# Kernel tuning notes

Measured on AMD Instinct MI355X. Metric: run time of the kernel, lower is better.

Reference implementation:

```python
import jax, jax.numpy as jnp
import numpy as np

E = 1024
BUCKET = 16
TAU = 0.75
ITERS = 8
SCALE = E ** -0.5
EPS = 1e-6


def _gumbel(rng, shape):
    u = jax.random.uniform(rng, shape, jnp.float32, 0.0, 1.0)
    return -jnp.log(-jnp.log(u + EPS) + EPS)


def _log_sinkhorn(log_alpha, n_iter):
    def body(i, la):
        la = la - jax.scipy.special.logsumexp(la, axis=-1, keepdims=True)
        la = la - jax.scipy.special.logsumexp(la, axis=-2, keepdims=True)
        return la
    return jnp.exp(jax.lax.fori_loop(0, n_iter, body, log_alpha))


def setup_inputs() -> dict:
    rng = jax.random.key(0)
    ks = jax.random.split(rng, 9)
    T, B, S = 4096, 8, 4096
    w = 0.02
    return {
        "query": jax.random.normal(ks[0], (T, B, E), jnp.float32),
        "key": jax.random.normal(ks[1], (S, B, E), jnp.float32),
        "value": jax.random.normal(ks[2], (S, B, E), jnp.float32),
        "wq": jax.random.normal(ks[3], (E, E), jnp.float32) * w,
        "bq": jnp.zeros((E,), jnp.float32),
        "wk": jax.random.normal(ks[4], (E, E), jnp.float32) * w,
        "bk": jnp.zeros((E,), jnp.float32),
        "wo": jax.random.normal(ks[5], (E, E), jnp.float32) * w,
        "bo": jnp.zeros((E,), jnp.float32),
    }


def reference(query, key, value, wq, bq, wk, bk, wo, bo):
    T, B, _ = query.shape
    S = key.shape[0]
    # projections (Linear: x @ W.T + b), move to (B, T, E)
    q = jnp.einsum('tbe,fe->btf', query, wq) + bq
    k = jnp.einsum('sbe,fe->bsf', key, wk) + bk
    v = jnp.transpose(value, (1, 0, 2))  # (B, S, E)
    nb, nkb = T // BUCKET, S // BUCKET
    # bucket aggregation: mean-pool q/k, flatten v buckets
    qb = q.reshape(B, nb, BUCKET, E).mean(axis=2)          # (B, nb, E)
    kb = k.reshape(B, nkb, BUCKET, E).mean(axis=2)         # (B, nkb, E)
    vb = v.reshape(B, nkb, BUCKET * E)                     # (B, nkb, BUCKET*E)
    # dot energy
    logits = jnp.einsum('bqe,bke->bqk', qb, kb) * SCALE    # (B, nb, nkb)
    log_alpha = logits
    # gumbel-sinkhorn (noise=True)
    g = _gumbel(jax.random.key(42), logits.shape)
    attn_weights = _log_sinkhorn((logits.astype(jnp.float32) + g) / TAU, ITERS)
    # attend on flattened buckets, then un-aggregate
    attn = jnp.einsum('bqk,bkd->bqd', attn_weights, vb)    # (B, nb, BUCKET*E)
    attn = attn.reshape(B, nb * BUCKET, E)
    attn = jnp.transpose(attn, (1, 0, 2))                  # (T, B, E)
    out = jnp.einsum('tbe,fe->tbf', attn, wo) + bo
    return out, attn_weights, log_alpha
```

## Files before the change

### kernel.cpp

```cpp
#include <hip/hip_runtime.h>


typedef float    f32x4 __attribute__((ext_vector_type(4)));
typedef _Float16 h4    __attribute__((ext_vector_type(4)));
typedef _Float16 h8    __attribute__((ext_vector_type(8)));

#define OUT_ELEMS 33554432
#define AW_ELEMS  524288

__device__ __forceinline__ void gload16(const void* g, void* l) {
  __builtin_amdgcn_global_load_lds((__attribute__((address_space(1))) void*)g,
                                   (__attribute__((address_space(3))) void*)l,
                                   16, 0, 0);
}

__global__ __launch_bounds__(256) void convw_k(const float* __restrict__ wq,
                                               const float* __restrict__ wk,
                                               const float* __restrict__ wo,
                                               _Float16* __restrict__ dst) {
  int which = blockIdx.y;
  const float* src = which == 0 ? wq : (which == 1 ? wk : wo);
  size_t idx = (size_t)blockIdx.x * 256 + threadIdx.x;
  f32x4 v = ((const f32x4*)src)[idx];
  ((h4*)(dst + (size_t)which * 1048576))[idx] = __builtin_convertvector(v, h4);
}

__global__ __launch_bounds__(256) void bucket_k(const float* __restrict__ q,
                                                const float* __restrict__ k,
                                                _Float16* __restrict__ qbar,
                                                _Float16* __restrict__ kbar) {
  const float* src = blockIdx.y ? k : q;
  _Float16* dst = blockIdx.y ? kbar : qbar;
  unsigned t = blockIdx.x * 256 + threadIdx.x;
  int e4 = t & 255, i = (t >> 8) & 255, b = t >> 16;
  const f32x4* p = (const f32x4*)(src + ((size_t)(i * 16) * 8 + b) * 1024) + e4;
  f32x4 acc = {0.f, 0.f, 0.f, 0.f};
  #pragma unroll
  for (int j = 0; j < 16; ++j) acc += p[j * 2048];
  acc *= 0.0625f;
  ((h4*)(dst + (size_t)(b * 256 + i) * 1024))[e4] = __builtin_convertvector(acc, h4);
}

__global__ __launch_bounds__(256) void vtrans_k(const float* __restrict__ v,
                                                _Float16* __restrict__ vt) {
  int bid = blockIdx.x;
  int kb = bid & 3, eb = (bid >> 2) & 15, j = (bid >> 6) & 15, b = bid >> 10;
  int k0 = kb * 64, e0 = eb * 64;
  __shared__ _Float16 tile[64][72];
  int t = threadIdx.x, r = t >> 2, qq = t & 3;
  const float* src = v + ((size_t)((k0 + r) * 16 + j) * 8 + b) * 1024 + e0;
  #pragma unroll
  for (int ii = 0; ii < 4; ++ii) {
    f32x4 x = ((const f32x4*)src)[qq + ii * 4];
    *(h4*)&tile[r][(qq + ii * 4) * 4] = __builtin_convertvector(x, h4);
  }
  __syncthreads();
  _Float16* dstp = vt + (((size_t)(b * 16 + j) * 1024 + e0 + r) * 256 + k0 + qq * 16);
  h8 o0, o1;
  #pragma unroll
  for (int kk = 0; kk < 8; ++kk) o0[kk] = tile[qq * 16 + kk][r];
  #pragma unroll
  for (int kk = 0; kk < 8; ++kk) o1[kk] = tile[qq * 16 + 8 + kk][r];
  *(h8*)dstp = o0;
  *(h8*)(dstp + 8) = o1;
}

__device__ __forceinline__ unsigned rotl32(unsigned x, int r) {
  return (x << r) | (x >> (32 - r));
}
__global__ __launch_bounds__(256) void gumbel_k(const float* __restrict__ logits,
                                                float* __restrict__ ebuf) {
  unsigned i = blockIdx.x * 256 + threadIdx.x;
  const unsigned k0 = 0u, k1 = 42u, k2 = 0u ^ 42u ^ 0x1BD11BDAu;
  unsigned x0 = 0u + k0, x1 = i + k1;
#define R4(a,b,c,d) \
  x0 += x1; x1 = rotl32(x1, a); x1 ^= x0; \
  x0 += x1; x1 = rotl32(x1, b); x1 ^= x0; \
  x0 += x1; x1 = rotl32(x1, c); x1 ^= x0; \
  x0 += x1; x1 = rotl32(x1, d); x1 ^= x0;
  R4(13,15,26,6)  x0 += k1; x1 += k2 + 1u;
  R4(17,29,16,24) x0 += k2; x1 += k0 + 2u;
  R4(13,15,26,6)  x0 += k0; x1 += k1 + 3u;
  R4(17,29,16,24) x0 += k1; x1 += k2 + 4u;
  R4(13,15,26,6)  x0 += k2; x1 += k0 + 5u;
#undef R4
  unsigned bits = x0 ^ x1;
  float u = __builtin_bit_cast(float, (bits >> 9) | 0x3f800000u) - 1.0f;
  float g = -logf(-logf(u + 1e-6f) + 1e-6f);
  ebuf[i] = __expf((logits[i] + g) / 0.75f);
}

__global__ __launch_bounds__(1024) void sink_rc_k(const float* __restrict__ ein,
                                                  float* __restrict__ attnw,
                                                  _Float16* __restrict__ wsh) {
  const int b = blockIdx.x;
  const int t = threadIdx.x;
  const int r = t >> 2, p = t & 3;
  const int k = t & 255, g = t >> 8;
  const float* Eb = ein + (size_t)b * 65536;
  const f32x4* Eb4 = (const f32x4*)Eb;

  __shared__ float ra[256];
  __shared__ float cb[256];
  __shared__ float part[4][256];
  if (t < 256) cb[t] = 1.0f;
  __syncthreads();

  const f32x4* cb4 = (const f32x4*)cb;

  for (int it = 0; it < 8; ++it) {
    float s = 0.f;
    #pragma unroll
    for (int i = 0; i < 16; ++i) {
      f32x4 e = Eb4[r * 64 + p * 16 + i];
      f32x4 c = cb4[p * 16 + i];
      f32x4 m = e * c;
      s += (m[0] + m[1]) + (m[2] + m[3]);
    }
    s += __shfl_xor(s, 1, 64);
    s += __shfl_xor(s, 2, 64);
    if (p == 0) ra[r] = 1.0f / s;
    __syncthreads();
    float s2 = 0.f;
    #pragma unroll 8
    for (int q2 = 0; q2 < 64; ++q2) {
      int row = g * 64 + q2;
      s2 += Eb[row * 256 + k] * ra[row];
    }
    part[g][k] = s2;
    __syncthreads();
    if (t < 256) {
      cb[t] = 1.0f / (part[0][t] + part[1][t] + part[2][t] + part[3][t]);
    }
    __syncthreads();
  }

  const float arow = ra[r];
  f32x4* aw = (f32x4*)(attnw + (size_t)b * 65536 + r * 256 + p * 64);
  h4* wh = (h4*)(wsh + (size_t)b * 65536 + r * 256 + p * 64);
  #pragma unroll
  for (int i = 0; i < 16; ++i) {
    f32x4 e = Eb4[r * 64 + p * 16 + i];
    f32x4 c = cb4[p * 16 + i];
    f32x4 w = e * c * arow;
    aw[i] = w;
    h4 hv;
    hv[0] = (_Float16)w[0]; hv[1] = (_Float16)w[1];
    hv[2] = (_Float16)w[2]; hv[3] = (_Float16)w[3];
    wh[i] = hv;
  }
}

template <int MODE>
__global__ __launch_bounds__(256) void gemm128(const _Float16* __restrict__ A,
                                               const _Float16* __restrict__ B,
                                               const float* __restrict__ bias,
                                               const float* __restrict__ bias2,
                                               void* __restrict__ out0,
                                               int K, int lda, int ldb) {
  const int tid = threadIdx.x, lane = tid & 63, w = tid >> 6;
  int bx = blockIdx.x, by = blockIdx.y, bz = blockIdx.z;
  if constexpr (MODE == 0) {
    int wid = ((bx & 7) << 4) + (bx >> 3);
    by = wid & 7; bx = wid >> 3;
  }
  if constexpr (MODE == 2) {
    int wid = ((bx & 7) << 8) + (bx >> 3);
    bz = wid >> 4; by = (wid >> 1) & 7; bx = wid & 1;
  }
  if constexpr (MODE == 3) {
    int wid = ((bx & 7) << 8) + (bx >> 3);
    by = wid & 7; bx = wid >> 3;
  }
  const int m0 = bx * 128, n0 = by * 128;
  const _Float16* Ab = A;
  const _Float16* Bb = B;
  const float* bs = bias;
  if constexpr (MODE == 0) {
    Ab += (size_t)bz * 2097152;
    Bb += (size_t)bz * 1048576;
    if (bz) bs = bias2;
  }
  if constexpr (MODE == 1) { Ab += (size_t)bz * 262144; Bb += (size_t)bz * 262144; }
  if constexpr (MODE == 2) { Ab += (size_t)(bz >> 4) * 65536; Bb += (size_t)bz * 262144; }
  __shared__ _Float16 lA[128 * 32];
  __shared__ _Float16 lB[128 * 32];
  f32x4 acc[4][4] = {};
  const int wm = (w >> 1) * 64, wn = (w & 1) * 64;
  const int fr = lane & 15, fk = (lane >> 4) * 8;
  const int q0 = tid, q1 = tid + 256;

  for (int kt = 0; kt < K; kt += 32) {
    __syncthreads();
    gload16(Ab + (size_t)(m0 + (q0 >> 2)) * lda + kt + (q0 & 3) * 8, &lA[(w * 64) * 8]);
    gload16(Ab + (size_t)(m0 + (q1 >> 2)) * lda + kt + (q1 & 3) * 8, &lA[(256 + w * 64) * 8]);
    gload16(Bb + (size_t)(n0 + (q0 >> 2)) * ldb + kt + (q0 & 3) * 8, &lB[(w * 64) * 8]);
    gload16(Bb + (size_t)(n0 + (q1 >> 2)) * ldb + kt + (q1 & 3) * 8, &lB[(256 + w * 64) * 8]);
    __syncthreads();
    h8 af[4], bf[4];
    #pragma unroll
    for (int i = 0; i < 4; ++i) {
      af[i] = *(const h8*)&lA[(wm + i * 16 + fr) * 32 + fk];
      bf[i] = *(const h8*)&lB[(wn + i * 16 + fr) * 32 + fk];
    }
    #pragma unroll
    for (int mi = 0; mi < 4; ++mi)
      #pragma unroll
      for (int ni = 0; ni < 4; ++ni)
        acc[mi][ni] = __builtin_amdgcn_mfma_f32_16x16x32_f16(af[mi], bf[ni], acc[mi][ni], 0, 0, 0);
  }

  const int er = (lane >> 4) * 4;
  #pragma unroll
  for (int mi = 0; mi < 4; ++mi) {
    #pragma unroll
    for (int ni = 0; ni < 4; ++ni) {
      #pragma unroll
      for (int r = 0; r < 4; ++r) {
        int row = m0 + wm + mi * 16 + er + r;
        int col = n0 + wn + ni * 16 + fr;
        float val = acc[mi][ni][r];
        if constexpr (MODE == 0) {
          ((_Float16*)out0)[(size_t)bz * 2097152 + (size_t)row * 1024 + col] =
              (_Float16)(val + bs[col]);
        } else if constexpr (MODE == 1) {
          ((float*)out0)[(size_t)bz * 65536 + row * 256 + col] = val * 0.03125f;
        } else if constexpr (MODE == 2) {
          int b = bz >> 4, j = bz & 15;
          ((_Float16*)out0)[((size_t)(b * 4096 + row * 16 + j)) * 1024 + col] = (_Float16)val;
        } else {
          int bb = row >> 12, t = row & 4095;
          ((float*)out0)[((size_t)t * 8 + bb) * 1024 + col] = val + bs[col];
        }
      }
    }
  }
}

extern "C" void kernel_launch(void* const* d_in, const int* in_sizes, int n_in,
                              void* d_out, int out_size, void* d_ws, size_t ws_size,
                              hipStream_t stream) {
  const float* query = (const float*)d_in[0];
  const float* key   = (const float*)d_in[1];
  const float* value = (const float*)d_in[2];
  const float* wq    = (const float*)d_in[3];
  const float* bq    = (const float*)d_in[4];
  const float* wk    = (const float*)d_in[5];
  const float* bk    = (const float*)d_in[6];
  const float* wo    = (const float*)d_in[7];
  const float* bo    = (const float*)d_in[8];

  float* out      = (float*)d_out;
  float* attnw    = out + OUT_ELEMS;
  float* logalpha = out + OUT_ELEMS + AW_ELEMS;

  char* ws = (char*)d_ws;
  const size_t MB = 1024 * 1024;
  _Float16* wqh   = (_Float16*)(ws + 0 * MB);
  _Float16* woh   = (_Float16*)(ws + 4 * MB);
  _Float16* qbar  = (_Float16*)(ws + 6 * MB);
  _Float16* kbar  = (_Float16*)(ws + 10 * MB);
  _Float16* qbh   = (_Float16*)(ws + 14 * MB);
  _Float16* kbh   = (_Float16*)(ws + 18 * MB);
  float*    ebuf  = (float*)(ws + 22 * MB);
  _Float16* wsh   = (_Float16*)(ws + 25 * MB);
  _Float16* vt    = (_Float16*)(ws + 26 * MB);
  _Float16* attnh = (_Float16*)(ws + 90 * MB);
  (void)in_sizes; (void)n_in; (void)out_size; (void)ws_size;

  convw_k<<<dim3(1024, 3), 256, 0, stream>>>(wq, wk, wo, wqh);
  bucket_k<<<dim3(2048, 2), 256, 0, stream>>>(query, key, qbar, kbar);
  vtrans_k<<<dim3(8192), 256, 0, stream>>>(value, vt);

  gemm128<0><<<dim3(128, 1, 2), 256, 0, stream>>>(qbar, wqh, bq, bk, qbh, 1024, 1024, 1024);
  gemm128<1><<<dim3(2, 2, 8), 256, 0, stream>>>(qbh, kbh, nullptr, nullptr, logalpha, 1024, 1024, 1024);

  gumbel_k<<<dim3(2048), 256, 0, stream>>>(logalpha, ebuf);
  sink_rc_k<<<dim3(8), 1024, 0, stream>>>(ebuf, attnw, wsh);

  gemm128<2><<<dim3(2048), 256, 0, stream>>>(wsh, vt, nullptr, nullptr, attnh, 256, 256, 256);
  gemm128<3><<<dim3(2048), 256, 0, stream>>>(attnh, woh, bo, nullptr, out, 1024, 1024, 1024);
}
```

Baseline: 377.9 us.

## Merge weight/bucket prep kernels and overlap V transpose with Sinkhorn

Fuses the weight-conversion and bucket-mean kernels into a single launch, and moves the V transpose into the Sinkhorn kernel as extra blocks. The Sinkhorn step runs on only 8 blocks, so the 2048 transpose blocks (four 256-thread sub-tiles per 1024-thread block) fill the otherwise idle CUs while it runs. This removes two launches and hides the transpose's memory traffic behind the latency-bound normalization. The cost is a larger shared allocation per block and a shared __syncthreads across the four sub-tiles.

```diff
diff --git a/kernel.cpp b/kernel.cpp
--- a/kernel.cpp
+++ b/kernel.cpp
@@ -14,55 +14,34 @@
                                    16, 0, 0);
 }
 
-__global__ __launch_bounds__(256) void convw_k(const float* __restrict__ wq,
-                                               const float* __restrict__ wk,
-                                               const float* __restrict__ wo,
-                                               _Float16* __restrict__ dst) {
-  int which = blockIdx.y;
-  const float* src = which == 0 ? wq : (which == 1 ? wk : wo);
-  size_t idx = (size_t)blockIdx.x * 256 + threadIdx.x;
-  f32x4 v = ((const f32x4*)src)[idx];
-  ((h4*)(dst + (size_t)which * 1048576))[idx] = __builtin_convertvector(v, h4);
-}
-
-__global__ __launch_bounds__(256) void bucket_k(const float* __restrict__ q,
-                                                const float* __restrict__ k,
-                                                _Float16* __restrict__ qbar,
-                                                _Float16* __restrict__ kbar) {
-  const float* src = blockIdx.y ? k : q;
-  _Float16* dst = blockIdx.y ? kbar : qbar;
-  unsigned t = blockIdx.x * 256 + threadIdx.x;
-  int e4 = t & 255, i = (t >> 8) & 255, b = t >> 16;
-  const f32x4* p = (const f32x4*)(src + ((size_t)(i * 16) * 8 + b) * 1024) + e4;
-  f32x4 acc = {0.f, 0.f, 0.f, 0.f};
-  #pragma unroll
-  for (int j = 0; j < 16; ++j) acc += p[j * 2048];
-  acc *= 0.0625f;
-  ((h4*)(dst + (size_t)(b * 256 + i) * 1024))[e4] = __builtin_convertvector(acc, h4);
-}
-
-__global__ __launch_bounds__(256) void vtrans_k(const float* __restrict__ v,
-                                                _Float16* __restrict__ vt) {
+__global__ __launch_bounds__(256) void cb_k(const float* __restrict__ wq,
+                                            const float* __restrict__ wk,
+                                            const float* __restrict__ wo,
+                                            _Float16* __restrict__ wdst,
+                                            const float* __restrict__ q,
+                                            const float* __restrict__ k,
+                                            _Float16* __restrict__ qbar,
+                                            _Float16* __restrict__ kbar) {
   int bid = blockIdx.x;
-  int kb = bid & 3, eb = (bid >> 2) & 15, j = (bid >> 6) & 15, b = bid >> 10;
-  int k0 = kb * 64, e0 = eb * 64;
-  __shared__ _Float16 tile[64][72];
-  int t = threadIdx.x, r = t >> 2, qq = t & 3;
-  const float* src = v + ((size_t)((k0 + r) * 16 + j) * 8 + b) * 1024 + e0;
-  #pragma unroll
-  for (int ii = 0; ii < 4; ++ii) {
-    f32x4 x = ((const f32x4*)src)[qq + ii * 4];
-    *(h4*)&tile[r][(qq + ii * 4) * 4] = __builtin_convertvector(x, h4);
-  }
-  __syncthreads();
-  _Float16* dstp = vt + (((size_t)(b * 16 + j) * 1024 + e0 + r) * 256 + k0 + qq * 16);
-  h8 o0, o1;
-  #pragma unroll
-  for (int kk = 0; kk < 8; ++kk) o0[kk] = tile[qq * 16 + kk][r];
-  #pragma unroll
-  for (int kk = 0; kk < 8; ++kk) o1[kk] = tile[qq * 16 + 8 + kk][r];
-  *(h8*)dstp = o0;
-  *(h8*)(dstp + 8) = o1;
+  if (bid < 3072) {
+    int which = bid >> 10;
+    const float* src = which == 0 ? wq : (which == 1 ? wk : wo);
+    size_t idx = (size_t)(bid & 1023) * 256 + threadIdx.x;
+    f32x4 v = ((const f32x4*)src)[idx];
+    ((h4*)(wdst + (size_t)which * 1048576))[idx] = __builtin_convertvector(v, h4);
+  } else {
+    int vb = bid - 3072;
+    const float* src = (vb >= 2048) ? k : q;
+    _Float16* dst = (vb >= 2048) ? kbar : qbar;
+    unsigned t = (unsigned)(vb & 2047) * 256 + threadIdx.x;
+    int e4 = t & 255, i = (t >> 8) & 255, b = t >> 16;
+    const f32x4* p = (const f32x4*)(src + ((size_t)(i * 16) * 8 + b) * 1024) + e4;
+    f32x4 acc = {0.f, 0.f, 0.f, 0.f};
+    #pragma unroll
+    for (int j = 0; j < 16; ++j) acc += p[j * 2048];
+    acc *= 0.0625f;
+    ((h4*)(dst + (size_t)(b * 256 + i) * 1024))[e4] = __builtin_convertvector(acc, h4);
+  }
 }
 
 __device__ __forceinline__ unsigned rotl32(unsigned x, int r) {
@@ -90,64 +69,89 @@
   ebuf[i] = __expf((logits[i] + g) / 0.75f);
 }
 
-__global__ __launch_bounds__(1024) void sink_rc_k(const float* __restrict__ ein,
-                                                  float* __restrict__ attnw,
-                                                  _Float16* __restrict__ wsh) {
-  const int b = blockIdx.x;
+__global__ __launch_bounds__(1024) void sinkvt_k(const float* __restrict__ ein,
+                                                 float* __restrict__ attnw,
+                                                 _Float16* __restrict__ wsh,
+                                                 const float* __restrict__ v,
+                                                 _Float16* __restrict__ vt) {
+  __shared__ __attribute__((aligned(16))) char smem[36864];
   const int t = threadIdx.x;
-  const int r = t >> 2, p = t & 3;
-  const int k = t & 255, g = t >> 8;
-  const float* Eb = ein + (size_t)b * 65536;
-  const f32x4* Eb4 = (const f32x4*)Eb;
-
-  __shared__ float ra[256];
-  __shared__ float cb[256];
-  __shared__ float part[4][256];
-  if (t < 256) cb[t] = 1.0f;
-  __syncthreads();
-
-  const f32x4* cb4 = (const f32x4*)cb;
-
-  for (int it = 0; it < 8; ++it) {
-    float s = 0.f;
+  if (blockIdx.x < 8) {
+    const int b = blockIdx.x;
+    const int r = t >> 2, p = t & 3;
+    const int k = t & 255, g = t >> 8;
+    const float* Eb = ein + (size_t)b * 65536;
+    const f32x4* Eb4 = (const f32x4*)Eb;
+    float* ra = (float*)smem;
+    float* cb = ra + 256;
+    float (*part)[256] = (float (*)[256])(cb + 256);
+    if (t < 256) cb[t] = 1.0f;
+    __syncthreads();
+    const f32x4* cb4 = (const f32x4*)cb;
+
+    for (int it = 0; it < 8; ++it) {
+      float s = 0.f;
+      #pragma unroll
+      for (int i = 0; i < 16; ++i) {
+        f32x4 e = Eb4[r * 64 + p * 16 + i];
+        f32x4 c = cb4[p * 16 + i];
+        f32x4 m = e * c;
+        s += (m[0] + m[1]) + (m[2] + m[3]);
+      }
+      s += __shfl_xor(s, 1, 64);
+      s += __shfl_xor(s, 2, 64);
+      if (p == 0) ra[r] = 1.0f / s;
+      __syncthreads();
+      float s2 = 0.f;
+      #pragma unroll 8
+      for (int q2 = 0; q2 < 64; ++q2) {
+        int row = g * 64 + q2;
+        s2 += Eb[row * 256 + k] * ra[row];
+      }
+      part[g][k] = s2;
+      __syncthreads();
+      if (t < 256) {
+        cb[t] = 1.0f / (part[0][t] + part[1][t] + part[2][t] + part[3][t]);
+      }
+      __syncthreads();
+    }
+
+    const float arow = ra[r];
+    f32x4* aw = (f32x4*)(attnw + (size_t)b * 65536 + r * 256 + p * 64);
+    h4* wh = (h4*)(wsh + (size_t)b * 65536 + r * 256 + p * 64);
     #pragma unroll
     for (int i = 0; i < 16; ++i) {
       f32x4 e = Eb4[r * 64 + p * 16 + i];
       f32x4 c = cb4[p * 16 + i];
-      f32x4 m = e * c;
-      s += (m[0] + m[1]) + (m[2] + m[3]);
-    }
-    s += __shfl_xor(s, 1, 64);
-    s += __shfl_xor(s, 2, 64);
-    if (p == 0) ra[r] = 1.0f / s;
-    __syncthreads();
-    float s2 = 0.f;
-    #pragma unroll 8
-    for (int q2 = 0; q2 < 64; ++q2) {
-      int row = g * 64 + q2;
-      s2 += Eb[row * 256 + k] * ra[row];
-    }
-    part[g][k] = s2;
-    __syncthreads();
-    if (t < 256) {
-      cb[t] = 1.0f / (part[0][t] + part[1][t] + part[2][t] + part[3][t]);
-    }
-    __syncthreads();
-  }
-
-  const float arow = ra[r];
-  f32x4* aw = (f32x4*)(attnw + (size_t)b * 65536 + r * 256 + p * 64);
-  h4* wh = (h4*)(wsh + (size_t)b * 65536 + r * 256 + p * 64);
-  #pragma unroll
-  for (int i = 0; i < 16; ++i) {
-    f32x4 e = Eb4[r * 64 + p * 16 + i];
-    f32x4 c = cb4[p * 16 + i];
-    f32x4 w = e * c * arow;
-    aw[i] = w;
-    h4 hv;
-    hv[0] = (_Float16)w[0]; hv[1] = (_Float16)w[1];
-    hv[2] = (_Float16)w[2]; hv[3] = (_Float16)w[3];
-    wh[i] = hv;
+      f32x4 w = e * c * arow;
+      aw[i] = w;
+      h4 hv;
+      hv[0] = (_Float16)w[0]; hv[1] = (_Float16)w[1];
+      hv[2] = (_Float16)w[2]; hv[3] = (_Float16)w[3];
+      wh[i] = hv;
+    }
+  } else {
+    const int s = t >> 8, t2 = t & 255;
+    int bid = (blockIdx.x - 8) * 4 + s;
+    _Float16 (*tile)[72] = (_Float16 (*)[72])(smem + s * 9216);
+    int kb = bid & 3, eb = (bid >> 2) & 15, j = (bid >> 6) & 15, b = bid >> 10;
+    int k0 = kb * 64, e0 = eb * 64;
+    int r = t2 >> 2, qq = t2 & 3;
+    const float* src = v + ((size_t)((k0 + r) * 16 + j) * 8 + b) * 1024 + e0;
+    #pragma unroll
+    for (int ii = 0; ii < 4; ++ii) {
+      f32x4 x = ((const f32x4*)src)[qq + ii * 4];
+      *(h4*)&tile[r][(qq + ii * 4) * 4] = __builtin_convertvector(x, h4);
+    }
+    __syncthreads();
+    _Float16* dstp = vt + (((size_t)(b * 16 + j) * 1024 + e0 + r) * 256 + k0 + qq * 16);
+    h8 o0, o1;
+    #pragma unroll
+    for (int kk = 0; kk < 8; ++kk) o0[kk] = tile[qq * 16 + kk][r];
+    #pragma unroll
+    for (int kk = 0; kk < 8; ++kk) o1[kk] = tile[qq * 16 + 8 + kk][r];
+    *(h8*)dstp = o0;
+    *(h8*)(dstp + 8) = o1;
   }
 }
 
@@ -268,15 +272,13 @@
   _Float16* attnh = (_Float16*)(ws + 90 * MB);
   (void)in_sizes; (void)n_in; (void)out_size; (void)ws_size;
 
-  convw_k<<<dim3(1024, 3), 256, 0, stream>>>(wq, wk, wo, wqh);
-  bucket_k<<<dim3(2048, 2), 256, 0, stream>>>(query, key, qbar, kbar);
-  vtrans_k<<<dim3(8192), 256, 0, stream>>>(value, vt);
+  cb_k<<<dim3(7168), 256, 0, stream>>>(wq, wk, wo, wqh, query, key, qbar, kbar);
 
   gemm128<0><<<dim3(128, 1, 2), 256, 0, stream>>>(qbar, wqh, bq, bk, qbh, 1024, 1024, 1024);
   gemm128<1><<<dim3(2, 2, 8), 256, 0, stream>>>(qbh, kbh, nullptr, nullptr, logalpha, 1024, 1024, 1024);
 
   gumbel_k<<<dim3(2048), 256, 0, stream>>>(logalpha, ebuf);
-  sink_rc_k<<<dim3(8), 1024, 0, stream>>>(ebuf, attnw, wsh);
+  sinkvt_k<<<dim3(2056), 1024, 0, stream>>>(ebuf, attnw, wsh, value, vt);
 
   gemm128<2><<<dim3(2048), 256, 0, stream>>>(wsh, vt, nullptr, nullptr, attnh, 256, 256, 256);
   gemm128<3><<<dim3(2048), 256, 0, stream>>>(attnh, woh, bo, nullptr, out, 1024, 1024, 1024);
```

Result: faster. 352.8 us (-6.6%).
